# Performance work log

Measured on AMD Instinct MI355X. Metric: run time of the kernel, lower is better.

The kernel has to match this reference:

```python
import jax, jax.numpy as jnp
import numpy as np

B, C, H, W = 2, 64, 256, 256
SIZE, STRIDE = 8, 4
NUMS = (H - SIZE) // STRIDE + 1          # 63 patches per axis
L = NUMS * NUMS                           # 3969 patches
K2 = SIZE * SIZE                          # 64 pixels per patch
EPS = 1e-05
TABLE = (2 * NUMS - 1) * (2 * NUMS - 1)   # relative-position bias table size


def _unfold_idx():
    # linear pixel index for each (kernel-offset k, patch l): [K2, L]
    i0 = np.arange(NUMS) * STRIDE
    j0 = np.arange(NUMS) * STRIDE
    kh = np.arange(SIZE)
    kw = np.arange(SIZE)
    r = kh[:, None, None, None] + i0[None, None, :, None]   # [S,1,N,1]
    c = kw[None, :, None, None] + j0[None, None, None, :]   # [1,S,1,N]
    return (r * W + c).reshape(K2, L)


def _rel_pos_index():
    ch = np.arange(NUMS)
    cw = np.arange(NUMS)
    coords = np.stack(np.meshgrid(ch, cw, indexing='ij'))   # [2,N,N]
    cf = coords.reshape(2, -1)                               # [2,L]
    rc = (cf[:, :, None] - cf[:, None, :]).transpose(1, 2, 0).astype(np.int64)
    rc[:, :, 0] += NUMS - 1
    rc[:, :, 1] += NUMS - 1
    rc[:, :, 0] *= 2 * NUMS - 1
    return rc.sum(-1)                                        # [L,L]


_IDX_NP = _unfold_idx()
_IDX = jnp.asarray(_IDX_NP)
_RPI = jnp.asarray(_rel_pos_index())
_count_np = np.zeros(H * W, np.float32)
np.add.at(_count_np, _IDX_NP.ravel(), 1.0)
_COUNT = jnp.asarray(_count_np.reshape(1, 1, H, W))


def setup_inputs() -> dict:
    key = jax.random.key(0)
    ks = jax.random.split(key, 9)
    x = jax.random.normal(ks[0], (B, C, H, W), dtype=jnp.float32)
    mask = jnp.round(jax.random.uniform(ks[1], (B, 1, H, W), dtype=jnp.float32))
    fg_gamma = 0.1 * jax.random.normal(ks[2], (C,), dtype=jnp.float32)
    fg_beta = 0.1 * jax.random.normal(ks[3], (C,), dtype=jnp.float32)
    bg_gamma = 0.1 * jax.random.normal(ks[4], (C,), dtype=jnp.float32)
    bg_beta = 0.1 * jax.random.normal(ks[5], (C,), dtype=jnp.float32)
    w_fore = 0.02 * jax.random.normal(ks[6], (C, C, K2), dtype=jnp.float32)
    w_back = 0.02 * jax.random.normal(ks[7], (C, C, K2), dtype=jnp.float32)
    rpb_table = 0.02 * jax.random.normal(ks[8], (TABLE,), dtype=jnp.float32)
    return {"x": x, "mask": mask, "fg_gamma": fg_gamma, "fg_beta": fg_beta,
            "bg_gamma": bg_gamma, "bg_beta": bg_beta,
            "w_fore": w_fore, "w_back": w_back, "rpb_table": rpb_table}


def _unfold(t):
    # [B,Ct,H,W] -> [B,Ct,L,K2]  (gather patch pixels)
    b, ct = t.shape[0], t.shape[1]
    return t.reshape(b, ct, H * W)[:, :, _IDX].transpose(0, 1, 3, 2)


def _patch_mean_std(region, m):
    # region [B,Ct,L,K2], m [B,1,L,K2] -> mu, 'std' (actually variance, per source)
    num = m.sum(-1)                                   # [B,1,L]
    mu = region.sum(-1) / (num + EPS)                 # [B,Ct,L]
    var = ((region - m * mu[..., None]) ** 2).sum(-1) / (num + EPS)
    return mu, var


def reference(x, mask, fg_gamma, fg_beta, bg_gamma, bg_beta, w_fore, w_back, rpb_table):
    # mask is already HxW -> nearest interpolate is identity
    invm = 1.0 - mask
    background = x * invm
    foreground = x * mask
    unorm_bg = (background * (1.0 + bg_gamma[None, :, None, None])
                + bg_beta[None, :, None, None]) * invm

    pb = _unfold(background)          # [B,C,L,K2]
    pf = _unfold(foreground)
    pm = _unfold(mask)                # [B,1,L,K2]

    mb, sb = _patch_mean_std(pb, 1.0 - pm)
    mf, sf = _patch_mean_std(pf, pm)

    in_b = (pb - mb[..., None]) / sb[..., None] * (1.0 - pm) + mb[..., None] * pm
    in_f = (pf - mf[..., None]) / sf[..., None] * pm + mf[..., None] * (1.0 - pm)

    tok_b = jnp.einsum('bclk,dck->bdl', in_b, w_back)   # [B,C,L]
    tok_f = jnp.einsum('bclk,dck->bdl', in_f, w_fore)

    bias = rpb_table[_RPI.reshape(-1)].reshape(L, L)
    S = jax.nn.softmax(jnp.einsum('bcl,bcm->blm', tok_f, tok_b) + bias[None], axis=-1)

    new_std = jnp.einsum('blm,bcm->bcl', S, sb)[..., None]   # [B,C,L,1]
    new_pf = in_f * new_std + new_std                        # (source uses new_std twice)

    # fold: scatter-add overlapping patches back, divide by coverage count
    flat = new_pf.transpose(0, 1, 3, 2).reshape(B, C, K2 * L)
    folded = jnp.zeros((B, C, H * W), x.dtype).at[:, :, _IDX.reshape(-1)].add(flat)
    new_fg = folded.reshape(B, C, H, W) / _COUNT

    new_fg = (new_fg * (1.0 + fg_gamma[None, :, None, None])
              + fg_beta[None, :, None, None]) * mask
    return new_fg + unorm_bg
```

## Files before the change

### kernel.cpp

```cpp
#include <hip/hip_runtime.h>
#include <stdint.h>

#define L_   3969
#define LP   3972
#define EPS_ 1e-5f
#define LOG2E 1.4426950408889634f
#define MH   6
#define IMR  11
#define PLANE 254208

#define OFF_MF   0
#define OFF_SF   508416
#define OFF_MB   1016832
#define OFF_SB   1525248
#define OFF_TOKF 2033664
#define OFF_TOKB 2542080
#define OFF_PACC 3050496
#define OFF_PM   6100992
#define OFF_PD   6148656
#define OFF_WT   6196320
#define PART_SLICE 1016832

#define OFF_A    2033664
#define OFF_B    2542080
#define OFF_C    4067328

typedef __attribute__((ext_vector_type(8))) short bf16x8;
typedef __attribute__((ext_vector_type(4))) float f32x4;

__device__ __forceinline__ uint16_t bf16_rne(float f) {
    uint32_t u = __float_as_uint(f);
    return (uint16_t)((u + 0x7FFFu + ((u >> 16) & 1u)) >> 16);
}
__device__ __forceinline__ void split_bf16(float v, uint16_t& h, uint16_t& l) {
    uint32_t u = __float_as_uint(v);
    uint32_t hu = u & 0xFFFF0000u;
    h = (uint16_t)(hu >> 16);
    l = bf16_rne(v - __uint_as_float(hu));
}
__device__ __forceinline__ uint4 pack8(const uint16_t* s) {
    uint4 r;
    r.x = (uint32_t)s[0] | ((uint32_t)s[1] << 16);
    r.y = (uint32_t)s[2] | ((uint32_t)s[3] << 16);
    r.z = (uint32_t)s[4] | ((uint32_t)s[5] << 16);
    r.w = (uint32_t)s[6] | ((uint32_t)s[7] << 16);
    return r;
}
__device__ __forceinline__ uint32_t pkhi2(float a, float b) {
    return (__float_as_uint(a) >> 16) | (__float_as_uint(b) & 0xFFFF0000u);
}
__device__ __forceinline__ uint32_t pklo2(float a, float b) {
    float ra = a - __uint_as_float(__float_as_uint(a) & 0xFFFF0000u);
    float rb = b - __uint_as_float(__float_as_uint(b) & 0xFFFF0000u);
    uint32_t r;
    asm("v_cvt_pk_bf16_f32 %0, %1, %2" : "=v"(r) : "v"(ra), "v"(rb));
    return r;
}

__global__ void k0_w2(const float* __restrict__ wf, const float* __restrict__ wb,
                      float* __restrict__ ws) {
    int c = blockIdx.x, t = blockIdx.y;
    const float* w = t ? wb : wf;
    uint16_t* w2 = (uint16_t*)(ws + OFF_WT);
    int tid = threadIdx.x;
    int lane = tid & 63, dq = tid >> 6;
    int d = dq * 16 + (lane & 15), quad = lane >> 4;
    for (int kci = 0; kci < 2; ++kci) {
        int k = kci * 32 + quad * 8;
        const float* src = w + (size_t)(d * 64 + c) * 64 + k;
        uint16_t hb[8], lb[8];
#pragma unroll
        for (int j = 0; j < 8; ++j) split_bf16(src[j], hb[j], lb[j]);
        size_t base = ((size_t)(((t * 64 + c) * 2 + kci) * 4 + dq) * 2) * 512 + lane * 8;
        *(uint4*)(w2 + base) = pack8(hb);
        *(uint4*)(w2 + base + 512) = pack8(lb);
    }
}

__global__ void k1_stats(const float* __restrict__ x, const float* __restrict__ mask,
                         float* __restrict__ ws) {
    int i = blockIdx.x, c = blockIdx.y, b = blockIdx.z;
    __shared__ float xs[8 * 256];
    __shared__ float ms[8 * 256];
    __shared__ float pS[5][256];
    int t = threadIdx.x;
    const float* xr = x + (((b * 64 + c) * 256) + i * 4) * 256;
    const float* mr = mask + (b * 256 + i * 4) * 256;
#pragma unroll
    for (int r = 0; r < 8; ++r) {
        xs[r * 256 + t] = xr[r * 256 + t];
        ms[r * 256 + t] = mr[r * 256 + t];
    }
    __syncthreads();
    int q = t >> 6, j = t & 63;
    float Sa = 0, Qa = 0, Sf = 0, Qf = 0, Nf = 0;
    if (j < 63) {
#pragma unroll
        for (int rr = 0; rr < 2; ++rr) {
            int base = (q * 2 + rr) * 256 + j * 4;
#pragma unroll
            for (int cc = 0; cc < 8; ++cc) {
                float v = xs[base + cc], m = ms[base + cc];
                Sa += v; Qa += v * v; Sf += v * m; Qf += v * v * m; Nf += m;
            }
        }
    }
    pS[0][t] = Sa; pS[1][t] = Qa; pS[2][t] = Sf; pS[3][t] = Qf; pS[4][t] = Nf;
    __syncthreads();
    if (q == 0 && j < 63) {
        Sa = pS[0][j] + pS[0][j + 64] + pS[0][j + 128] + pS[0][j + 192];
        Qa = pS[1][j] + pS[1][j + 64] + pS[1][j + 128] + pS[1][j + 192];
        Sf = pS[2][j] + pS[2][j + 64] + pS[2][j + 128] + pS[2][j + 192];
        Qf = pS[3][j] + pS[3][j + 64] + pS[3][j + 128] + pS[3][j + 192];
        Nf = pS[4][j] + pS[4][j + 64] + pS[4][j + 128] + pS[4][j + 192];
        float nb = 64.0f - Nf;
        float muf = Sf / (Nf + EPS_);
        float vaf = (Qf - 2.f * muf * Sf + Nf * muf * muf) / (Nf + EPS_);
        float Sb = Sa - Sf, Qb = Qa - Qf;
        float mub = Sb / (nb + EPS_);
        float vab = (Qb - 2.f * mub * Sb + nb * mub * mub) / (nb + EPS_);
        int idx = (b * 64 + c) * LP + i * 63 + j;
        ws[OFF_MF + idx] = muf; ws[OFF_SF + idx] = vaf;
        ws[OFF_MB + idx] = mub; ws[OFF_SB + idx] = vab;
    }
}

__global__ __launch_bounds__(256)
void k2_tok(const float* __restrict__ x, const float* __restrict__ mask,
            const float* __restrict__ wsc, float* __restrict__ ws) {
    int il = blockIdx.x, kc = blockIdx.y, b = blockIdx.z;
    int tid = threadIdx.x;
    int jl = tid & 63;
    int q = tid >> 6;
    __shared__ uint16_t IN[2][4 * 64 * 72];
    const uint16_t* w2 = (const uint16_t*)(wsc + OFF_WT);

    bool lv = jl < 63;
    int lg = il * 63 + jl;

    uint32_t mbits[2] = {0u, 0u};
    if (lv) {
#pragma unroll
        for (int oi = 0; oi < 2; ++oi) {
            int o = q + oi * 4;
            const float* mp = mask + (size_t)b * 65536 + (il * 4 + o) * 256 + jl * 4;
            float4 m0 = *(const float4*)mp;
            float4 m1 = *(const float4*)(mp + 4);
            uint32_t bits = 0;
            bits |= (m0.x != 0.f) ? 1u : 0u;  bits |= (m0.y != 0.f) ? 2u : 0u;
            bits |= (m0.z != 0.f) ? 4u : 0u;  bits |= (m0.w != 0.f) ? 8u : 0u;
            bits |= (m1.x != 0.f) ? 16u : 0u; bits |= (m1.y != 0.f) ? 32u : 0u;
            bits |= (m1.z != 0.f) ? 64u : 0u; bits |= (m1.w != 0.f) ? 128u : 0u;
            mbits[oi] = bits;
        }
    }

    f32x4 acc[2][2][2];
#pragma unroll
    for (int t = 0; t < 2; ++t)
#pragma unroll
        for (int i2 = 0; i2 < 2; ++i2)
#pragma unroll
            for (int j2 = 0; j2 < 2; ++j2) acc[t][i2][j2] = (f32x4)(0.f);

    int lane = tid & 63;
    int quad = lane >> 4;
    int c16 = lane & 15;
    int wd = q >> 1, wl = q & 1;
    int c0 = kc * 16;

    float4 xa[2][2];
    if (!lv) {
        xa[0][0] = xa[0][1] = xa[1][0] = xa[1][1] = make_float4(0.f, 0.f, 0.f, 0.f);
    }
    float muF = 0.f, vaF = 1.f, muB = 0.f, vaB = 1.f;

#define K2_LOADCH(cc)                                                                \
    do {                                                                             \
        if (lv) {                                                                    \
            int si = (b * 64 + (cc)) * LP + lg;                                      \
            muF = wsc[OFF_MF + si]; vaF = wsc[OFF_SF + si];                          \
            muB = wsc[OFF_MB + si]; vaB = wsc[OFF_SB + si];                          \
            const float* xp0 = x + (size_t)(b * 64 + (cc)) * 65536 + (il * 4 + q) * 256 + jl * 4; \
            xa[0][0] = *(const float4*)xp0;                                          \
            xa[0][1] = *(const float4*)(xp0 + 4);                                    \
            xa[1][0] = *(const float4*)(xp0 + 1024);                                 \
            xa[1][1] = *(const float4*)(xp0 + 1028);                                 \
        }                                                                            \
    } while (0)

#define K2_PACKSTORE(bufsel)                                                         \
    do {                                                                             \
        float invF = lv ? (1.0f / vaF) : 0.f;                                        \
        float invB = lv ? (1.0f / vaB) : 0.f;                                        \
        float cmF = lv ? muF : 0.f;                                                  \
        float cmB = lv ? muB : 0.f;                                                  \
        _Pragma("unroll")                                                            \
        for (int oi = 0; oi < 2; ++oi) {                                             \
            float xv[8];                                                             \
            xv[0] = xa[oi][0].x; xv[1] = xa[oi][0].y;                                \
            xv[2] = xa[oi][0].z; xv[3] = xa[oi][0].w;                                \
            xv[4] = xa[oi][1].x; xv[5] = xa[oi][1].y;                                \
            xv[6] = xa[oi][1].z; xv[7] = xa[oi][1].w;                                \
            float fv[8], bv[8];                                                      \
            _Pragma("unroll")                                                        \
            for (int j = 0; j < 8; ++j) {                                            \
                bool mf = (mbits[oi] >> j) & 1;                                      \
                float v = xv[j];                                                     \
                fv[j] = mf ? (v - cmF) * invF : cmF;                                 \
                bv[j] = mf ? cmB : (v - cmB) * invB;                                 \
            }                                                                        \
            uint4 FH, FL, BH, BL;                                                    \
            FH.x = pkhi2(fv[0], fv[1]); FH.y = pkhi2(fv[2], fv[3]);                  \
            FH.z = pkhi2(fv[4], fv[5]); FH.w = pkhi2(fv[6], fv[7]);                  \
            FL.x = pklo2(fv[0], fv[1]); FL.y = pklo2(fv[2], fv[3]);                  \
            FL.z = pklo2(fv[4], fv[5]); FL.w = pklo2(fv[6], fv[7]);                  \
            BH.x = pkhi2(bv[0], bv[1]); BH.y = pkhi2(bv[2], bv[3]);                  \
            BH.z = pkhi2(bv[4], bv[5]); BH.w = pkhi2(bv[6], bv[7]);                  \
            BL.x = pklo2(bv[0], bv[1]); BL.y = pklo2(bv[2], bv[3]);                  \
            BL.z = pklo2(bv[4], bv[5]); BL.w = pklo2(bv[6], bv[7]);                  \
            uint16_t* dst = &IN[bufsel][jl * 72 + (q + oi * 4) * 8];                 \
            *(uint4*)(dst)         = FH;                                             \
            *(uint4*)(dst + 4608)  = FL;                                             \
            *(uint4*)(dst + 9216)  = BH;                                             \
            *(uint4*)(dst + 13824) = BL;                                             \
        }                                                                            \
    } while (0)

#define K2_MFMA(bufi, cch)                                                           \
    do {                                                                             \
        _Pragma("unroll")                                                            \
        for (int t = 0; t < 2; ++t) {                                                \
            _Pragma("unroll")                                                        \
            for (int kci = 0; kci < 2; ++kci) {                                      \
                bf16x8 Ah[2], Al[2];                                                 \
                _Pragma("unroll")                                                    \
                for (int dqi = 0; dqi < 2; ++dqi) {                                  \
                    const uint16_t* ab = w2 +                                        \
                        ((size_t)(((t * 64 + (cch)) * 2 + kci) * 4 + (wd * 2 + dqi)) * 2) * 512 + lane * 8; \
                    Ah[dqi] = *(const bf16x8*)ab;                                    \
                    Al[dqi] = *(const bf16x8*)(ab + 512);                            \
                }                                                                    \
                _Pragma("unroll")                                                    \
                for (int lt = 0; lt < 2; ++lt) {                                     \
                    const uint16_t* bp = &IN[bufi][(t * 2) * 4608 +                  \
                        (wl * 32 + lt * 16 + c16) * 72 + kci * 32 + quad * 8];       \
                    bf16x8 Bh = *(const bf16x8*)bp;                                  \
                    bf16x8 Bl = *(const bf16x8*)(bp + 4608);                         \
                    _Pragma("unroll")                                                \
                    for (int dqi = 0; dqi < 2; ++dqi) {                              \
                        acc[t][dqi][lt] = __builtin_amdgcn_mfma_f32_16x16x32_bf16(Ah[dqi], Bh, acc[t][dqi][lt], 0, 0, 0); \
                        acc[t][dqi][lt] = __builtin_amdgcn_mfma_f32_16x16x32_bf16(Ah[dqi], Bl, acc[t][dqi][lt], 0, 0, 0); \
                        acc[t][dqi][lt] = __builtin_amdgcn_mfma_f32_16x16x32_bf16(Al[dqi], Bh, acc[t][dqi][lt], 0, 0, 0); \
                    }                                                                \
                }                                                                    \
            }                                                                        \
        }                                                                            \
    } while (0)

    K2_LOADCH(c0);
    K2_PACKSTORE(0);
    K2_LOADCH(c0 + 1);
    __syncthreads();

#pragma unroll 2
    for (int ci = 0; ci < 16; ++ci) {
        int cur = ci & 1;
        if (ci < 15) {
            K2_PACKSTORE(cur ^ 1);
            if (ci < 14) K2_LOADCH(c0 + ci + 2);
        }
        K2_MFMA(cur, c0 + ci);
        __syncthreads();
    }
#undef K2_LOADCH
#undef K2_PACKSTORE
#undef K2_MFMA

    float* ST = (float*)&IN[0][0];
#pragma unroll
    for (int t = 0; t < 2; ++t) {
        __syncthreads();
#pragma unroll
        for (int dqi = 0; dqi < 2; ++dqi)
#pragma unroll
            for (int lt = 0; lt < 2; ++lt)
#pragma unroll
                for (int r = 0; r < 4; ++r)
                    ST[(wl * 32 + lt * 16 + c16) * 68 + (wd * 2 + dqi) * 16 + quad * 4 + r] =
                        acc[t][dqi][lt][r];
        __syncthreads();
        float* dst = ws + OFF_TOKF + (size_t)kc * PART_SLICE + ((t * 2 + b) * (size_t)LP) * 64;
        int d4 = (tid & 15) * 4;
#pragma unroll
        for (int pass = 0; pass < 4; ++pass) {
            int l = pass * 16 + (tid >> 4);
            if (l < 63)
                *(float4*)&dst[(size_t)(il * 63 + l) * 64 + d4] = *(float4*)&ST[l * 68 + d4];
        }
    }
}

__global__ void k2r_reduce(float* __restrict__ ws) {
    size_t e = ((size_t)blockIdx.x * 256 + threadIdx.x) * 4;
    float4 a0 = *(float4*)&ws[OFF_TOKF + e];
    float4 a1 = *(float4*)&ws[OFF_TOKF + PART_SLICE + e];
    float4 a2 = *(float4*)&ws[OFF_TOKF + 2 * PART_SLICE + e];
    float4 a3 = *(float4*)&ws[OFF_TOKF + 3 * PART_SLICE + e];
    float s0 = a0.x + a1.x + a2.x + a3.x;
    float s1 = a0.y + a1.y + a2.y + a3.y;
    float s2 = a0.z + a1.z + a2.z + a3.z;
    float s3 = a0.w + a1.w + a2.w + a3.w;
    int tb = (int)(e / (size_t)PLANE);
    int idx = (int)(e - (size_t)tb * PLANE);
    int t = tb >> 1, b = tb & 1;
    uint16_t* pl = (uint16_t*)(ws + (t ? OFF_WT : OFF_SB));
    uint2 hv, lv;
    hv.x = pkhi2(s0, s1); hv.y = pkhi2(s2, s3);
    lv.x = pklo2(s0, s1); lv.y = pklo2(s2, s3);
    *(uint2*)&pl[(size_t)(b * 2 + 0) * PLANE + idx] = hv;
    *(uint2*)&pl[(size_t)(b * 2 + 1) * PLANE + idx] = lv;
}

__global__ void k1s_sb(float* __restrict__ ws) {
    int im = blockIdx.x, b = blockIdx.y;
    int tid = threadIdx.x;
    int c = tid >> 2, mm = (tid & 3) * 16;
    const float* src = ws + OFF_SB + ((size_t)b * 64 + c) * LP + im * 63 + mm;
    uint16_t sv[16];
#pragma unroll
    for (int u = 0; u < 16; ++u)
        sv[u] = (mm + u < 63) ? bf16_rne(src[u]) : (uint16_t)0;
    uint16_t* dst = (uint16_t*)(ws + OFF_MB) + (((size_t)b * 63 + im) * 64 + c) * 64 + mm;
    *(uint4*)(dst) = pack8(sv);
    *(uint4*)(dst + 8) = pack8(sv + 8);
}

__global__ __launch_bounds__(256)
void k3_attn(const float* __restrict__ wsc, const float* __restrict__ rpb,
             float* __restrict__ ws) {
    int il = blockIdx.x, imc = blockIdx.y, b = blockIdx.z;
    int tid = threadIdx.x;
    int w = tid >> 6, lane = tid & 63;
    int c16 = lane & 15, quad = lane >> 4;

    __shared__ uint16_t TFh[64 * 72], TFl[64 * 72];
    __shared__ uint16_t TBh[64 * 72];
    __shared__ uint16_t TBl[64 * 72];
    __shared__ uint16_t SB[64 * 72];
    __shared__ float bias_r[128];

    const uint16_t* tfp = (const uint16_t*)(wsc + OFF_SB);
    const uint16_t* tbp = (const uint16_t*)(wsc + OFF_WT);
    const uint16_t* TFH = tfp + (size_t)(b * 2 + 0) * PLANE;
    const uint16_t* TFL = tfp + (size_t)(b * 2 + 1) * PLANE;
    const uint16_t* TBH = tbp + (size_t)(b * 2 + 0) * PLANE;
    const uint16_t* TBL = tbp + (size_t)(b * 2 + 1) * PLANE;
    const uint16_t* sbb = (const uint16_t*)(wsc + OFF_MB);

    {
        int jl = tid >> 2, cc = (tid & 3) * 16;
        uint4 h0 = make_uint4(0u,0u,0u,0u), h1 = h0, l0 = h0, l1 = h0;
        if (jl < 63) {
            const uint16_t* sh = TFH + (size_t)(il * 63 + jl) * 64 + cc;
            const uint16_t* sl = TFL + (size_t)(il * 63 + jl) * 64 + cc;
            h0 = *(const uint4*)sh; h1 = *(const uint4*)(sh + 8);
            l0 = *(const uint4*)sl; l1 = *(const uint4*)(sl + 8);
        }
        *(uint4*)&TFh[jl * 72 + cc] = h0; *(uint4*)&TFh[jl * 72 + cc + 8] = h1;
        *(uint4*)&TFl[jl * 72 + cc] = l0; *(uint4*)&TFl[jl * 72 + cc + 8] = l1;
    }

    float mrun[4] = {-1e30f, -1e30f, -1e30f, -1e30f};
    float drun[4] = {0.f, 0.f, 0.f, 0.f};
    f32x4 acc2[4];
#pragma unroll
    for (int ct = 0; ct < 4; ++ct) acc2[ct] = (f32x4)(0.f);

    int im0 = imc * IMR;
    int im1 = min(63, im0 + IMR);

    int jms = tid >> 2, ccs = (tid & 3) * 16;
    uint4 rTH0, rTH1, rTL0, rTL1, rS0, rS1;
    float rBias;

#define K3_PREFETCH(imv)                                                              \
    do {                                                                              \
        if (jms < 63) {                                                               \
            const uint16_t* sh_ = TBH + (size_t)((imv) * 63 + jms) * 64 + ccs;        \
            const uint16_t* sl_ = TBL + (size_t)((imv) * 63 + jms) * 64 + ccs;        \
            rTH0 = *(const uint4*)sh_; rTH1 = *(const uint4*)(sh_ + 8);               \
            rTL0 = *(const uint4*)sl_; rTL1 = *(const uint4*)(sl_ + 8);               \
        } else {                                                                      \
            rTH0 = rTH1 = rTL0 = rTL1 = make_uint4(0u,0u,0u,0u);                      \
        }                                                                             \
        const uint16_t* ss_ = sbb + (((size_t)b * 63 + (imv)) * 64 + jms) * 64 + ccs; \
        rS0 = *(const uint4*)ss_; rS1 = *(const uint4*)(ss_ + 8);                     \
        rBias = (tid < 125) ? rpb[(il - (imv) + 62) * 125 + tid] : 0.f;               \
    } while (0)

    K3_PREFETCH(im0);

    for (int im = im0; im < im1; ++im) {
        __syncthreads();
        *(uint4*)&TBh[jms * 72 + ccs] = rTH0; *(uint4*)&TBh[jms * 72 + ccs + 8] = rTH1;
        *(uint4*)&TBl[jms * 72 + ccs] = rTL0; *(uint4*)&TBl[jms * 72 + ccs + 8] = rTL1;
        *(uint4*)&SB[jms * 72 + ccs]  = rS0;  *(uint4*)&SB[jms * 72 + ccs + 8]  = rS1;
        if (tid < 128) bias_r[tid] = rBias;
        if (im + 1 < im1) K3_PREFETCH(im + 1);
        __syncthreads();

        f32x4 Z[4];
#pragma unroll
        for (int jt = 0; jt < 4; ++jt) Z[jt] = (f32x4)(0.f);
#pragma unroll
        for (int kk = 0; kk < 2; ++kk) {
            bf16x8 Ah = *(bf16x8*)&TFh[(w * 16 + c16) * 72 + kk * 32 + quad * 8];
            bf16x8 Al = *(bf16x8*)&TFl[(w * 16 + c16) * 72 + kk * 32 + quad * 8];
#pragma unroll
            for (int jt = 0; jt < 4; ++jt) {
                bf16x8 Bh = *(bf16x8*)&TBh[(jt * 16 + c16) * 72 + kk * 32 + quad * 8];
                bf16x8 Bl = *(bf16x8*)&TBl[(jt * 16 + c16) * 72 + kk * 32 + quad * 8];
                Z[jt] = __builtin_amdgcn_mfma_f32_16x16x32_bf16(Ah, Bh, Z[jt], 0, 0, 0);
                Z[jt] = __builtin_amdgcn_mfma_f32_16x16x32_bf16(Ah, Bl, Z[jt], 0, 0, 0);
                Z[jt] = __builtin_amdgcn_mfma_f32_16x16x32_bf16(Al, Bh, Z[jt], 0, 0, 0);
            }
        }
        float zv[4][4];
#pragma unroll
        for (int jt = 0; jt < 4; ++jt) {
            int jmz = jt * 16 + c16;
#pragma unroll
            for (int r = 0; r < 4; ++r) {
                int i = w * 16 + quad * 4 + r;
                zv[jt][r] = (jmz == 63) ? -1e30f : (Z[jt][r] + bias_r[i - jmz + 62]);
            }
        }
        float alphav[4];
        uint16_t pb[4][4];
#pragma unroll
        for (int r = 0; r < 4; ++r) {
            float v = fmaxf(fmaxf(zv[0][r], zv[1][r]), fmaxf(zv[2][r], zv[3][r]));
            v = fmaxf(v, __shfl_xor(v, 1));
            v = fmaxf(v, __shfl_xor(v, 2));
            v = fmaxf(v, __shfl_xor(v, 4));
            v = fmaxf(v, __shfl_xor(v, 8));
            float mnew = fmaxf(mrun[r], v);
            alphav[r] = exp2f((mrun[r] - mnew) * LOG2E);
            float s = 0.f;
#pragma unroll
            for (int jt = 0; jt < 4; ++jt) {
                float p = exp2f((zv[jt][r] - mnew) * LOG2E);
                uint16_t h = bf16_rne(p);
                pb[jt][r] = h;
                s += __uint_as_float((uint32_t)h << 16);
            }
            s += __shfl_xor(s, 1); s += __shfl_xor(s, 2);
            s += __shfl_xor(s, 4); s += __shfl_xor(s, 8);
            drun[r] = drun[r] * alphav[r] + s;
            mrun[r] = mnew;
        }
#pragma unroll
        for (int ct = 0; ct < 4; ++ct)
#pragma unroll
            for (int r = 0; r < 4; ++r) acc2[ct][r] *= alphav[r];

        __syncthreads();
#pragma unroll
        for (int jt = 0; jt < 4; ++jt)
#pragma unroll
            for (int r = 0; r < 4; ++r)
                TBh[(w * 16 + quad * 4 + r) * 72 + jt * 16 + c16] = pb[jt][r];
        __syncthreads();

#pragma unroll
        for (int kk = 0; kk < 2; ++kk) {
            bf16x8 Pf = *(bf16x8*)&TBh[(w * 16 + c16) * 72 + kk * 32 + quad * 8];
#pragma unroll
            for (int ct = 0; ct < 4; ++ct) {
                bf16x8 Sf = *(bf16x8*)&SB[(ct * 16 + c16) * 72 + kk * 32 + quad * 8];
                acc2[ct] = __builtin_amdgcn_mfma_f32_16x16x32_bf16(Pf, Sf, acc2[ct], 0, 0, 0);
            }
        }
    }

    float* PA = ws + OFF_PACC + ((imc * 2 + b) * (size_t)LP) * 64;
#pragma unroll
    for (int r = 0; r < 4; ++r) {
        int i = w * 16 + quad * 4 + r;
        if (i < 63) {
            int rl = il * 63 + i;
#pragma unroll
            for (int ct = 0; ct < 4; ++ct)
                PA[(size_t)rl * 64 + ct * 16 + c16] = acc2[ct][r];
            if (c16 == 0) {
                ws[OFF_PM + (imc * 2 + b) * LP + rl] = mrun[r];
                ws[OFF_PD + (imc * 2 + b) * LP + rl] = drun[r];
            }
        }
    }
#undef K3_PREFETCH
}

__global__ void k3b_merge(float* __restrict__ ws) {
    int b = blockIdx.y;
    int l = blockIdx.x * 4 + (threadIdx.x >> 6);
    int c = threadIdx.x & 63;
    if (l >= L_) return;
    float M = -1e30f;
#pragma unroll
    for (int p = 0; p < MH; ++p)
        M = fmaxf(M, ws[OFF_PM + (p * 2 + b) * LP + l]);
    float denom = 0.f, num = 0.f;
#pragma unroll
    for (int p = 0; p < MH; ++p) {
        float w = exp2f((ws[OFF_PM + (p * 2 + b) * LP + l] - M) * LOG2E);
        denom += ws[OFF_PD + (p * 2 + b) * LP + l] * w;
        num += ws[OFF_PACC + ((p * 2 + b) * (size_t)LP + l) * 64 + c] * w;
    }
    ws[OFF_PACC + (b * (size_t)LP + l) * 64 + c] = num / denom;
}

__global__ void k3c_coef(float* __restrict__ ws) {
    int b = blockIdx.y;
    int bl = blockIdx.x;
    int tid = threadIdx.x;
    __shared__ float T[3][4][65];
    int ls = tid >> 6, c = tid & 63;
    int l = bl * 4 + ls;
    float ns = ws[OFF_PACC + ((size_t)b * LP + l) * 64 + c];
    float mf = ws[OFF_MF + (size_t)(b * 64 + c) * LP + l];
    float sf = ws[OFF_SF + (size_t)(b * 64 + c) * LP + l];
    float a = ns / sf;
    T[0][ls][c] = a;
    T[1][ls][c] = ns - mf * a;
    T[2][ls][c] = ns * (mf + 1.f);
    __syncthreads();
    int c2 = tid >> 2, l2 = tid & 3;
    size_t o = (size_t)(b * 64 + c2) * LP + bl * 4 + l2;
    ws[OFF_A + o] = T[0][l2][c2];
    ws[OFF_B + o] = T[1][l2][c2];
    ws[OFF_C + o] = T[2][l2][c2];
}

__global__ void k4_fold(const float* __restrict__ x, const float* __restrict__ mask,
                        const float* __restrict__ fg_g, const float* __restrict__ fg_b,
                        const float* __restrict__ bg_g, const float* __restrict__ bg_b,
                        const float* __restrict__ wsc, float* __restrict__ out) {
    int gid = blockIdx.x * 256 + threadIdx.x;
    int col = gid & 255, r = (gid >> 8) & 255, c = (gid >> 16) & 63, b = gid >> 22;
    float xv = x[gid];
    float m = mask[b * 65536 + r * 256 + col];
    int imin = (r >= 4) ? ((r - 4) >> 2) : 0;
    int imax = min(62, r >> 2);
    int jmin = (col >= 4) ? ((col - 4) >> 2) : 0;
    int jmax = min(62, col >> 2);
    bool fi = imax > imin, fj = jmax > jmin;
    int l00 = imin * 63 + jmin;
    const float* Aa = wsc + OFF_A + (size_t)(b * 64 + c) * LP;
    const float* Ba = wsc + OFF_B + (size_t)(b * 64 + c) * LP;
    const float* Ca = wsc + OFF_C + (size_t)(b * 64 + c) * LP;
    float a00 = Aa[l00],      b00 = Ba[l00],      c00 = Ca[l00];
    float a01 = Aa[l00 + 1],  b01 = Ba[l00 + 1],  c01 = Ca[l00 + 1];
    float a10 = Aa[l00 + 63], b10 = Ba[l00 + 63], c10 = Ca[l00 + 63];
    float a11 = Aa[l00 + 64], b11 = Ba[l00 + 64], c11 = Ca[l00 + 64];
    bool fij = fi && fj;
    float SA = a00 + (fj ? a01 : 0.f) + (fi ? a10 : 0.f) + (fij ? a11 : 0.f);
    float SBv = b00 + (fj ? b01 : 0.f) + (fi ? b10 : 0.f) + (fij ? b11 : 0.f);
    float SCv = c00 + (fj ? c01 : 0.f) + (fi ? c10 : 0.f) + (fij ? c11 : 0.f);
    float folded = (m != 0.f) ? (xv * SA + SBv) : SCv;
    float rc = (fi ? 0.5f : 1.f) * (fj ? 0.5f : 1.f);
    float invm = 1.f - m;
    float ub = (xv * invm * (1.f + bg_g[c]) + bg_b[c]) * invm;
    float nf = (folded * rc * (1.f + fg_g[c]) + fg_b[c]) * m;
    out[gid] = nf + ub;
}

extern "C" void kernel_launch(void* const* d_in, const int* in_sizes, int n_in,
                              void* d_out, int out_size, void* d_ws, size_t ws_size,
                              hipStream_t stream) {
    const float* x    = (const float*)d_in[0];
    const float* mask = (const float*)d_in[1];
    const float* fg_g = (const float*)d_in[2];
    const float* fg_b = (const float*)d_in[3];
    const float* bg_g = (const float*)d_in[4];
    const float* bg_b = (const float*)d_in[5];
    const float* wf   = (const float*)d_in[6];
    const float* wb   = (const float*)d_in[7];
    const float* rpb  = (const float*)d_in[8];
    float* ws = (float*)d_ws;
    float* out = (float*)d_out;

    k0_w2<<<dim3(64, 2), 256, 0, stream>>>(wf, wb, ws);
    k1_stats<<<dim3(63, 64, 2), 256, 0, stream>>>(x, mask, ws);
    k2_tok<<<dim3(63, 4, 2), 256, 0, stream>>>(x, mask, ws, ws);
    k1s_sb<<<dim3(63, 2), 256, 0, stream>>>(ws);
    k2r_reduce<<<dim3(993), 256, 0, stream>>>(ws);
    k3_attn<<<dim3(63, MH, 2), 256, 0, stream>>>(ws, rpb, ws);
    k3b_merge<<<dim3(993, 2), 256, 0, stream>>>(ws);
    k3c_coef<<<dim3(993, 2), 256, 0, stream>>>(ws);
    k4_fold<<<dim3(32768), 256, 0, stream>>>(x, mask, fg_g, fg_b, bg_g, bg_b, ws, out);
}
```

Baseline: 255.0 us.

## Hold Q fragments in registers and transpose QK^T so softmax runs per lane

The attention kernel now keeps the query (TF) bf16 hi/lo fragments in registers instead of staging them in shared memory. It computes the score tile transposed (K·Q) so each lane owns one query row, which reduces the row max/sum reductions to two cross-quad shuffles. P is written to a dedicated per-wave LDS buffer with packed stores, which removes two __syncthreads per iteration. It also adds a launch_bounds occupancy hint of 4. The intended savings are LDS footprint, barrier stalls and shuffle work, at the cost of extra register pressure and an intra-wave LDS dependency that relies only on a compiler memory fence.

```diff
diff --git a/kernel.cpp b/kernel.cpp
--- a/kernel.cpp
+++ b/kernel.cpp
@@ -336,7 +336,7 @@
     *(uint4*)(dst + 8) = pack8(sv + 8);
 }
 
-__global__ __launch_bounds__(256)
+__global__ __launch_bounds__(256, 4)
 void k3_attn(const float* __restrict__ wsc, const float* __restrict__ rpb,
              float* __restrict__ ws) {
     int il = blockIdx.x, imc = blockIdx.y, b = blockIdx.z;
@@ -344,10 +344,10 @@
     int w = tid >> 6, lane = tid & 63;
     int c16 = lane & 15, quad = lane >> 4;
 
-    __shared__ uint16_t TFh[64 * 72], TFl[64 * 72];
     __shared__ uint16_t TBh[64 * 72];
     __shared__ uint16_t TBl[64 * 72];
     __shared__ uint16_t SB[64 * 72];
+    __shared__ uint16_t P[64 * 72];
     __shared__ float bias_r[128];
 
     const uint16_t* tfp = (const uint16_t*)(wsc + OFF_SB);
@@ -358,21 +358,15 @@
     const uint16_t* TBL = tbp + (size_t)(b * 2 + 1) * PLANE;
     const uint16_t* sbb = (const uint16_t*)(wsc + OFF_MB);
 
-    {
-        int jl = tid >> 2, cc = (tid & 3) * 16;
-        uint4 h0 = make_uint4(0u,0u,0u,0u), h1 = h0, l0 = h0, l1 = h0;
-        if (jl < 63) {
-            const uint16_t* sh = TFH + (size_t)(il * 63 + jl) * 64 + cc;
-            const uint16_t* sl = TFL + (size_t)(il * 63 + jl) * 64 + cc;
-            h0 = *(const uint4*)sh; h1 = *(const uint4*)(sh + 8);
-            l0 = *(const uint4*)sl; l1 = *(const uint4*)(sl + 8);
-        }
-        *(uint4*)&TFh[jl * 72 + cc] = h0; *(uint4*)&TFh[jl * 72 + cc + 8] = h1;
-        *(uint4*)&TFl[jl * 72 + cc] = l0; *(uint4*)&TFl[jl * 72 + cc + 8] = l1;
-    }
-
-    float mrun[4] = {-1e30f, -1e30f, -1e30f, -1e30f};
-    float drun[4] = {0.f, 0.f, 0.f, 0.f};
+    int qrow = il * 63 + w * 16 + c16;
+    bf16x8 Qh[2], Ql[2];
+#pragma unroll
+    for (int kk = 0; kk < 2; ++kk) {
+        Qh[kk] = *(const bf16x8*)&TFH[(size_t)qrow * 64 + kk * 32 + quad * 8];
+        Ql[kk] = *(const bf16x8*)&TFL[(size_t)qrow * 64 + kk * 32 + quad * 8];
+    }
+
+    float mrun = -1e30f, drun = 0.f;
     f32x4 acc2[4];
 #pragma unroll
     for (int ct = 0; ct < 4; ++ct) acc2[ct] = (f32x4)(0.f);
@@ -401,6 +395,8 @@
 
     K3_PREFETCH(im0);
 
+    int ibias = w * 16 + c16 + 62 - quad * 4;
+
     for (int im = im0; im < im1; ++im) {
         __syncthreads();
         *(uint4*)&TBh[jms * 72 + ccs] = rTH0; *(uint4*)&TBh[jms * 72 + ccs + 8] = rTH1;
@@ -414,74 +410,85 @@
 #pragma unroll
         for (int jt = 0; jt < 4; ++jt) Z[jt] = (f32x4)(0.f);
 #pragma unroll
+        for (int jt = 0; jt < 4; ++jt) {
+#pragma unroll
+            for (int kk = 0; kk < 2; ++kk) {
+                bf16x8 Kh = *(bf16x8*)&TBh[(jt * 16 + c16) * 72 + kk * 32 + quad * 8];
+                bf16x8 Kl = *(bf16x8*)&TBl[(jt * 16 + c16) * 72 + kk * 32 + quad * 8];
+                Z[jt] = __builtin_amdgcn_mfma_f32_16x16x32_bf16(Kh, Qh[kk], Z[jt], 0, 0, 0);
+                Z[jt] = __builtin_amdgcn_mfma_f32_16x16x32_bf16(Kh, Ql[kk], Z[jt], 0, 0, 0);
+                Z[jt] = __builtin_amdgcn_mfma_f32_16x16x32_bf16(Kl, Qh[kk], Z[jt], 0, 0, 0);
+            }
+        }
+
+        float zv[4][4];
+#pragma unroll
+        for (int jt = 0; jt < 4; ++jt)
+#pragma unroll
+            for (int r = 0; r < 4; ++r) {
+                int m = jt * 16 + quad * 4 + r;
+                int bi = ibias - jt * 16 - r;
+                bi = bi < 0 ? 0 : bi;
+                zv[jt][r] = (m == 63) ? -1e30f : (Z[jt][r] + bias_r[bi]);
+            }
+
+        float a0 = fmaxf(zv[0][0], zv[0][1]), a1 = fmaxf(zv[0][2], zv[0][3]);
+        float a2 = fmaxf(zv[1][0], zv[1][1]), a3 = fmaxf(zv[1][2], zv[1][3]);
+        float a4 = fmaxf(zv[2][0], zv[2][1]), a5 = fmaxf(zv[2][2], zv[2][3]);
+        float a6 = fmaxf(zv[3][0], zv[3][1]), a7 = fmaxf(zv[3][2], zv[3][3]);
+        a0 = fmaxf(a0, a1); a2 = fmaxf(a2, a3); a4 = fmaxf(a4, a5); a6 = fmaxf(a6, a7);
+        float vmax = fmaxf(fmaxf(a0, a2), fmaxf(a4, a6));
+        vmax = fmaxf(vmax, __shfl_xor(vmax, 16));
+        vmax = fmaxf(vmax, __shfl_xor(vmax, 32));
+        float mnew = fmaxf(mrun, vmax);
+        float alpha = exp2f((mrun - mnew) * LOG2E);
+        uint16_t pb[4][4];
+        float sv[8];
+#pragma unroll
+        for (int jt = 0; jt < 4; ++jt) {
+            float p0 = exp2f((zv[jt][0] - mnew) * LOG2E);
+            float p1 = exp2f((zv[jt][1] - mnew) * LOG2E);
+            float p2 = exp2f((zv[jt][2] - mnew) * LOG2E);
+            float p3 = exp2f((zv[jt][3] - mnew) * LOG2E);
+            uint16_t h0 = bf16_rne(p0), h1 = bf16_rne(p1);
+            uint16_t h2 = bf16_rne(p2), h3 = bf16_rne(p3);
+            pb[jt][0] = h0; pb[jt][1] = h1; pb[jt][2] = h2; pb[jt][3] = h3;
+            sv[jt * 2]     = __uint_as_float((uint32_t)h0 << 16) + __uint_as_float((uint32_t)h1 << 16);
+            sv[jt * 2 + 1] = __uint_as_float((uint32_t)h2 << 16) + __uint_as_float((uint32_t)h3 << 16);
+        }
+        float s = ((sv[0] + sv[1]) + (sv[2] + sv[3])) + ((sv[4] + sv[5]) + (sv[6] + sv[7]));
+        s += __shfl_xor(s, 16);
+        s += __shfl_xor(s, 32);
+        drun = drun * alpha + s;
+        mrun = mnew;
+
+        float alphav[4];
+#pragma unroll
+        for (int r = 0; r < 4; ++r) alphav[r] = __shfl(alpha, quad * 4 + r, 16);
+#pragma unroll
+        for (int ct = 0; ct < 4; ++ct)
+#pragma unroll
+            for (int r = 0; r < 4; ++r) acc2[ct][r] *= alphav[r];
+
+#pragma unroll
+        for (int jt = 0; jt < 4; ++jt) {
+            uint2 pw;
+            pw.x = (uint32_t)pb[jt][0] | ((uint32_t)pb[jt][1] << 16);
+            pw.y = (uint32_t)pb[jt][2] | ((uint32_t)pb[jt][3] << 16);
+            *(uint2*)&P[(w * 16 + c16) * 72 + jt * 16 + quad * 4] = pw;
+        }
+        asm volatile("" ::: "memory");
+
+#pragma unroll
         for (int kk = 0; kk < 2; ++kk) {
-            bf16x8 Ah = *(bf16x8*)&TFh[(w * 16 + c16) * 72 + kk * 32 + quad * 8];
-            bf16x8 Al = *(bf16x8*)&TFl[(w * 16 + c16) * 72 + kk * 32 + quad * 8];
-#pragma unroll
-            for (int jt = 0; jt < 4; ++jt) {
-                bf16x8 Bh = *(bf16x8*)&TBh[(jt * 16 + c16) * 72 + kk * 32 + quad * 8];
-                bf16x8 Bl = *(bf16x8*)&TBl[(jt * 16 + c16) * 72 + kk * 32 + quad * 8];
-                Z[jt] = __builtin_amdgcn_mfma_f32_16x16x32_bf16(Ah, Bh, Z[jt], 0, 0, 0);
-                Z[jt] = __builtin_amdgcn_mfma_f32_16x16x32_bf16(Ah, Bl, Z[jt], 0, 0, 0);
-                Z[jt] = __builtin_amdgcn_mfma_f32_16x16x32_bf16(Al, Bh, Z[jt], 0, 0, 0);
-            }
-        }
-        float zv[4][4];
-#pragma unroll
-        for (int jt = 0; jt < 4; ++jt) {
-            int jmz = jt * 16 + c16;
-#pragma unroll
-            for (int r = 0; r < 4; ++r) {
-                int i = w * 16 + quad * 4 + r;
-                zv[jt][r] = (jmz == 63) ? -1e30f : (Z[jt][r] + bias_r[i - jmz + 62]);
-            }
-        }
-        float alphav[4];
-        uint16_t pb[4][4];
-#pragma unroll
-        for (int r = 0; r < 4; ++r) {
-            float v = fmaxf(fmaxf(zv[0][r], zv[1][r]), fmaxf(zv[2][r], zv[3][r]));
-            v = fmaxf(v, __shfl_xor(v, 1));
-            v = fmaxf(v, __shfl_xor(v, 2));
-            v = fmaxf(v, __shfl_xor(v, 4));
-            v = fmaxf(v, __shfl_xor(v, 8));
-            float mnew = fmaxf(mrun[r], v);
-            alphav[r] = exp2f((mrun[r] - mnew) * LOG2E);
-            float s = 0.f;
-#pragma unroll
-            for (int jt = 0; jt < 4; ++jt) {
-                float p = exp2f((zv[jt][r] - mnew) * LOG2E);
-                uint16_t h = bf16_rne(p);
-                pb[jt][r] = h;
-                s += __uint_as_float((uint32_t)h << 16);
-            }
-            s += __shfl_xor(s, 1); s += __shfl_xor(s, 2);
-            s += __shfl_xor(s, 4); s += __shfl_xor(s, 8);
-            drun[r] = drun[r] * alphav[r] + s;
-            mrun[r] = mnew;
-        }
-#pragma unroll
-        for (int ct = 0; ct < 4; ++ct)
-#pragma unroll
-            for (int r = 0; r < 4; ++r) acc2[ct][r] *= alphav[r];
-
-        __syncthreads();
-#pragma unroll
-        for (int jt = 0; jt < 4; ++jt)
-#pragma unroll
-            for (int r = 0; r < 4; ++r)
-                TBh[(w * 16 + quad * 4 + r) * 72 + jt * 16 + c16] = pb[jt][r];
-        __syncthreads();
-
-#pragma unroll
-        for (int kk = 0; kk < 2; ++kk) {
-            bf16x8 Pf = *(bf16x8*)&TBh[(w * 16 + c16) * 72 + kk * 32 + quad * 8];
+            bf16x8 Pf = *(bf16x8*)&P[(w * 16 + c16) * 72 + kk * 32 + quad * 8];
 #pragma unroll
             for (int ct = 0; ct < 4; ++ct) {
                 bf16x8 Sf = *(bf16x8*)&SB[(ct * 16 + c16) * 72 + kk * 32 + quad * 8];
                 acc2[ct] = __builtin_amdgcn_mfma_f32_16x16x32_bf16(Pf, Sf, acc2[ct], 0, 0, 0);
             }
         }
+        asm volatile("" ::: "memory");
     }
 
     float* PA = ws + OFF_PACC + ((imc * 2 + b) * (size_t)LP) * 64;
@@ -493,10 +500,14 @@
 #pragma unroll
             for (int ct = 0; ct < 4; ++ct)
                 PA[(size_t)rl * 64 + ct * 16 + c16] = acc2[ct][r];
-            if (c16 == 0) {
-                ws[OFF_PM + (imc * 2 + b) * LP + rl] = mrun[r];
-                ws[OFF_PD + (imc * 2 + b) * LP + rl] = drun[r];
-            }
+        }
+    }
+    if (quad == 0) {
+        int i = w * 16 + c16;
+        if (i < 63) {
+            int rl = il * 63 + i;
+            ws[OFF_PM + (imc * 2 + b) * LP + rl] = mrun;
+            ws[OFF_PD + (imc * 2 + b) * LP + rl] = drun;
         }
     }
 #undef K3_PREFETCH
```

Measured after the change: 246.1 us. 1.04x faster.
